# Kernel tuning notes

Measured on AMD Instinct MI355X. Metric: run time of the kernel, lower is better.

The kernel has to match this reference:

```python
import jax, jax.numpy as jnp
import numpy as np

NEG = -1000000.0  # mask fill value used by the torch module


def setup_inputs() -> dict:
    key = jax.random.key(0)
    k1, k2, k3, k4 = jax.random.split(key, 4)
    B, L, D = 64, 1024, 64
    return {
        "queries": jax.random.normal(k1, (B, L, D), dtype=jnp.float32),
        "keys": jax.random.normal(k2, (B, L, D), dtype=jnp.float32),
        "values": jax.random.normal(k3, (B, L, D), dtype=jnp.float32),
        "valid_lens": jax.random.randint(k4, (B,), 1, 1024, dtype=jnp.int32),
    }


def reference(queries, keys, values, valid_lens):
    d = queries.shape[-1]
    # [B, Lq, Lk] attention scores
    scores = jnp.einsum("bqd,bkd->bqk", queries, keys) / jnp.sqrt(jnp.asarray(d, queries.dtype))
    Lk = scores.shape[-1]
    # sequence mask: key positions >= valid_len are filled with NEG (per batch)
    col = jnp.arange(Lk)  # [Lk]
    mask = col[None, None, :] >= valid_lens[:, None, None]  # [B, 1, Lk] -> broadcasts over q
    scores = jnp.where(mask, NEG, scores)
    attn = jax.nn.softmax(scores, axis=-1)
    # dropout p=0.0 (eval) -> identity
    return jnp.einsum("bqk,bkd->bqd", attn, values)
```

## Files before the change

kernel.cpp:

```cpp
#include <hip/hip_runtime.h>
#include <math.h>


typedef __attribute__((ext_vector_type(4))) float f32x4;
typedef __attribute__((ext_vector_type(8))) short bf16x8;
typedef __attribute__((ext_vector_type(8))) unsigned short u16x8;
typedef __attribute__((ext_vector_type(4))) unsigned short u16x4;

constexpr int Bn = 64, Ln = 1024, Dn = 64;
constexpr float QSCALE = 0.125f * 1.44269504088896340736f;
constexpr float DEFER_THR = 10.0f;

__device__ inline unsigned short f2bf(float x) {
    unsigned int u = __float_as_uint(x);
    return (unsigned short)((u + 0x7fffu + ((u >> 16) & 1u)) >> 16);
}

__global__ __launch_bounds__(256) void flash_attn(
    const float* __restrict__ Q, const float* __restrict__ K,
    const float* __restrict__ V, const int* __restrict__ VL,
    float* __restrict__ O)
{
    __shared__ unsigned short kls[2][64 * 64];
    __shared__ unsigned short vls[2][64 * 64];
    __shared__ unsigned short plds[4][16 * 64];

    const int tid = threadIdx.x;
    const int w = tid >> 6, l = tid & 63;
    const int lg = l >> 4, ln = l & 15;
    const int b = blockIdx.x >> 4;
    const int qt = blockIdx.x & 15;
    const int qbase = qt * 64 + w * 16;
    const int valid = VL[b];
    const int nkt = (valid + 63) >> 6;

    const float* Kbase = K + (size_t)b * Ln * Dn;
    const float* Vbase = V + (size_t)b * Ln * Dn;

    bf16x8 bq0, bq1;
    {
        const f32x4* qp = reinterpret_cast<const f32x4*>(Q + ((size_t)b * Ln + qbase + ln) * Dn);
        f32x4 q0 = qp[lg * 2], q1 = qp[lg * 2 + 1], q2 = qp[8 + lg * 2], q3 = qp[8 + lg * 2 + 1];
        #pragma unroll
        for (int j = 0; j < 4; ++j) {
            bq0[j]     = (short)f2bf(q0[j] * QSCALE);
            bq0[j + 4] = (short)f2bf(q1[j] * QSCALE);
            bq1[j]     = (short)f2bf(q2[j] * QSCALE);
            bq1[j + 4] = (short)f2bf(q3[j] * QSCALE);
        }
    }

    const int kr = tid >> 2, kc = (tid & 3) * 16;
    const int vd = l, vk0 = w * 16;

    f32x4 kpre[4];
    float vpre[16];

    char* const kls0 = reinterpret_cast<char*>(kls[0]);
    char* const kls1 = reinterpret_cast<char*>(kls[1]);
    char* const vls0 = reinterpret_cast<char*>(vls[0]);
    char* const vls1 = reinterpret_cast<char*>(vls[1]);
    char* const pwb  = reinterpret_cast<char*>(plds[w]);

    const int kb = kr * 128 + kc * 2, ksw = (kr & 7) << 4;
    const int vb = vd * 128 + vk0 * 2, vsw = (vd & 7) << 4;

    auto stage_write = [&](int p) {
        char* kd = p ? kls1 : kls0;
        char* vd_ = p ? vls1 : vls0;
        u16x8 c0, c1;
        #pragma unroll
        for (int j = 0; j < 4; ++j) {
            c0[j]     = f2bf(kpre[0][j]);  c0[j + 4] = f2bf(kpre[1][j]);
            c1[j]     = f2bf(kpre[2][j]);  c1[j + 4] = f2bf(kpre[3][j]);
        }
        *reinterpret_cast<u16x8*>(kd + ((kb)      ^ ksw)) = c0;
        *reinterpret_cast<u16x8*>(kd + ((kb + 16) ^ ksw)) = c1;
        u16x8 v0, v1;
        #pragma unroll
        for (int j = 0; j < 8; ++j) { v0[j] = f2bf(vpre[j]); v1[j] = f2bf(vpre[j + 8]); }
        *reinterpret_cast<u16x8*>(vd_ + ((vb)      ^ vsw)) = v0;
        *reinterpret_cast<u16x8*>(vd_ + ((vb + 16) ^ vsw)) = v1;
    };

    {
        const f32x4* kp = reinterpret_cast<const f32x4*>(Kbase + (size_t)kr * Dn + kc);
        #pragma unroll
        for (int i = 0; i < 4; ++i) kpre[i] = kp[i];
        const float* vp = Vbase + (size_t)vk0 * Dn + vd;
        #pragma unroll
        for (int i = 0; i < 16; ++i) vpre[i] = vp[(size_t)i * Dn];
    }
    stage_write(0);
    __syncthreads();

    f32x4 acc[4] = {{0.f,0.f,0.f,0.f},{0.f,0.f,0.f,0.f},{0.f,0.f,0.f,0.f},{0.f,0.f,0.f,0.f}};
    float mrow = -1e30f;
    float lrow = 0.f;

    int p = 0;
    for (int kt = 0; kt < nkt; ++kt, p ^= 1) {
        const bool has_next = (kt + 1 < nkt);
        char* kcur = p ? kls1 : kls0;
        char* vcur = p ? vls1 : vls0;

        if (has_next) {
            const f32x4* kp = reinterpret_cast<const f32x4*>(Kbase + (size_t)((kt + 1) * 64 + kr) * Dn + kc);
            #pragma unroll
            for (int i = 0; i < 4; ++i) kpre[i] = kp[i];
            const float* vp = Vbase + (size_t)((kt + 1) * 64 + vk0) * Dn + vd;
            #pragma unroll
            for (int i = 0; i < 16; ++i) vpre[i] = vp[(size_t)i * Dn];
        }

        f32x4 st[4] = {{0.f,0.f,0.f,0.f},{0.f,0.f,0.f,0.f},{0.f,0.f,0.f,0.f},{0.f,0.f,0.f,0.f}};
        #pragma unroll
        for (int t = 0; t < 4; ++t) {
            const int r = 16 * t + ln, rsw = (r & 7) << 4;
            bf16x8 ak0 = *reinterpret_cast<const bf16x8*>(kcur + ((r * 128 + lg * 16)      ^ rsw));
            st[t] = __builtin_amdgcn_mfma_f32_16x16x32_bf16(ak0, bq0, st[t], 0, 0, 0);
            bf16x8 ak1 = *reinterpret_cast<const bf16x8*>(kcur + ((r * 128 + lg * 16 + 64) ^ rsw));
            st[t] = __builtin_amdgcn_mfma_f32_16x16x32_bf16(ak1, bq1, st[t], 0, 0, 0);
        }

        const int kb0 = kt * 64 + lg * 4;
        if (kt * 64 + 64 > valid) {
            #pragma unroll
            for (int t = 0; t < 4; ++t)
                #pragma unroll
                for (int j = 0; j < 4; ++j)
                    if (kb0 + 16 * t + j >= valid) st[t][j] = -1e30f;
        }

        float mx;
        {
            float a0 = fmaxf(fmaxf(st[0][0], st[0][1]), fmaxf(st[0][2], st[0][3]));
            float a1 = fmaxf(fmaxf(st[1][0], st[1][1]), fmaxf(st[1][2], st[1][3]));
            float a2 = fmaxf(fmaxf(st[2][0], st[2][1]), fmaxf(st[2][2], st[2][3]));
            float a3 = fmaxf(fmaxf(st[3][0], st[3][1]), fmaxf(st[3][2], st[3][3]));
            mx = fmaxf(fmaxf(a0, a1), fmaxf(a2, a3));
            mx = fmaxf(mx, __shfl_xor(mx, 16, 64));
            mx = fmaxf(mx, __shfl_xor(mx, 32, 64));
        }

        if (__any(mx - mrow > DEFER_THR)) {
            const float mn = fmaxf(mrow, mx);
            const float rs = exp2f(mrow - mn);
            mrow = mn;
            lrow *= rs;
            #pragma unroll
            for (int j = 0; j < 4; ++j) {
                const float rsj = __shfl(rs, lg * 4 + j, 64);
                #pragma unroll
                for (int t = 0; t < 4; ++t) acc[t][j] *= rsj;
            }
        }

        float rsum = 0.f;
        const int psw = (ln & 7) << 4;
        #pragma unroll
        for (int t = 0; t < 4; ++t) {
            u16x4 pk;
            #pragma unroll
            for (int j = 0; j < 4; ++j) {
                const float pv = exp2f(st[t][j] - mrow);
                rsum += pv;
                pk[j] = f2bf(pv);
            }
            *reinterpret_cast<u16x4*>(pwb + ((ln * 128 + 32 * t + 8 * lg) ^ psw)) = pk;
        }
        rsum += __shfl_xor(rsum, 16, 64);
        rsum += __shfl_xor(rsum, 32, 64);
        lrow += rsum;

        #pragma unroll
        for (int s = 0; s < 2; ++s) {
            bf16x8 pa = *reinterpret_cast<const bf16x8*>(pwb + ((ln * 128 + lg * 16 + 64 * s) ^ psw));
            #pragma unroll
            for (int t = 0; t < 4; ++t) {
                const int r = 16 * t + ln, rsw = (r & 7) << 4;
                bf16x8 bv = *reinterpret_cast<const bf16x8*>(vcur + ((r * 128 + lg * 16 + 64 * s) ^ rsw));
                acc[t] = __builtin_amdgcn_mfma_f32_16x16x32_bf16(pa, bv, acc[t], 0, 0, 0);
            }
        }

        if (has_next) stage_write(p ^ 1);
        __syncthreads();
    }

    const float invl = 1.0f / lrow;
    float inv[4];
    #pragma unroll
    for (int j = 0; j < 4; ++j) inv[j] = __shfl(invl, lg * 4 + j, 64);
    float* Orow = O + ((size_t)b * Ln + qbase) * Dn;
    #pragma unroll
    for (int t = 0; t < 4; ++t) {
        #pragma unroll
        for (int j = 0; j < 4; ++j) {
            const int q = lg * 4 + j;
            const int d = 16 * t + ln;
            Orow[(size_t)q * Dn + d] = acc[t][j] * inv[j];
        }
    }
}

extern "C" void kernel_launch(void* const* d_in, const int* in_sizes, int n_in,
                              void* d_out, int out_size, void* d_ws, size_t ws_size,
                              hipStream_t stream) {
    const float* Q = (const float*)d_in[0];
    const float* K = (const float*)d_in[1];
    const float* V = (const float*)d_in[2];
    const int* VL = (const int*)d_in[3];
    float* O = (float*)d_out;
    flash_attn<<<Bn * 16, 256, 0, stream>>>(Q, K, V, VL, O);
}
```

Measured before the change: 127.2 us.

## Schedule batches longest-first and permute K rows for wider P stores

Each block ranks the 64 batches by valid length using wave shuffles and maps blockIdx through a scrambled permutation, so the longest batches start first and the variable-length tail is balanced across CUs. Separately, K rows are written to shared memory with a permuted row order, so each lane's score outputs become key-contiguous. That allows the P tile to be written with two 128-bit LDS stores instead of four 64-bit ones, and the mask index is updated to match. The cost is a per-block 64-iteration ranking loop and an extra barrier at kernel start.

New measurement: 137.5 us. 1.08x slower.

```diff
diff --git a/kernel.cpp b/kernel.cpp
--- a/kernel.cpp
+++ b/kernel.cpp
@@ -5,7 +5,6 @@
 typedef __attribute__((ext_vector_type(4))) float f32x4;
 typedef __attribute__((ext_vector_type(8))) short bf16x8;
 typedef __attribute__((ext_vector_type(8))) unsigned short u16x8;
-typedef __attribute__((ext_vector_type(4))) unsigned short u16x4;
 
 constexpr int Bn = 64, Ln = 1024, Dn = 64;
 constexpr float QSCALE = 0.125f * 1.44269504088896340736f;
@@ -24,12 +23,26 @@
     __shared__ unsigned short kls[2][64 * 64];
     __shared__ unsigned short vls[2][64 * 64];
     __shared__ unsigned short plds[4][16 * 64];
+    __shared__ int order_s[64];
 
     const int tid = threadIdx.x;
     const int w = tid >> 6, l = tid & 63;
     const int lg = l >> 4, ln = l & 15;
-    const int b = blockIdx.x >> 4;
-    const int qt = blockIdx.x & 15;
+
+    {
+        const int vme = VL[l];
+        int rank = 0;
+        for (int i = 0; i < 64; ++i) {
+            const int vi = __shfl(vme, i, 64);
+            rank += (vi > vme) || (vi == vme && i < l);
+        }
+        if (w == 0) order_s[rank] = l;
+    }
+    __syncthreads();
+
+    const int r = (633 * blockIdx.x) & 1023;
+    const int b = order_s[r >> 4];
+    const int qt = r & 15;
     const int qbase = qt * 64 + w * 16;
     const int valid = VL[b];
     const int nkt = (valid + 63) >> 6;
@@ -51,6 +64,7 @@
     }
 
     const int kr = tid >> 2, kc = (tid & 3) * 16;
+    const int sr = ((kr & 0xC) << 2) | ((kr >> 2) & 0xC) | (kr & 3);
     const int vd = l, vk0 = w * 16;
 
     f32x4 kpre[4];
@@ -62,12 +76,13 @@
     char* const vls1 = reinterpret_cast<char*>(vls[1]);
     char* const pwb  = reinterpret_cast<char*>(plds[w]);
 
-    const int kb = kr * 128 + kc * 2, ksw = (kr & 7) << 4;
+    const int kb = sr * 128 + kc * 2, ksw = (sr & 7) << 4;
     const int vb = vd * 128 + vk0 * 2, vsw = (vd & 7) << 4;
-
-    auto stage_write = [&](int p) {
-        char* kd = p ? kls1 : kls0;
-        char* vd_ = p ? vls1 : vls0;
+    const int psw = (ln & 7) << 4;
+
+    auto stage_write = [&](int pbuf) {
+        char* kd = pbuf ? kls1 : kls0;
+        char* vdst = pbuf ? vls1 : vls0;
         u16x8 c0, c1;
         #pragma unroll
         for (int j = 0; j < 4; ++j) {
@@ -79,8 +94,8 @@
         u16x8 v0, v1;
         #pragma unroll
         for (int j = 0; j < 8; ++j) { v0[j] = f2bf(vpre[j]); v1[j] = f2bf(vpre[j + 8]); }
-        *reinterpret_cast<u16x8*>(vd_ + ((vb)      ^ vsw)) = v0;
-        *reinterpret_cast<u16x8*>(vd_ + ((vb + 16) ^ vsw)) = v1;
+        *reinterpret_cast<u16x8*>(vdst + ((vb)      ^ vsw)) = v0;
+        *reinterpret_cast<u16x8*>(vdst + ((vb + 16) ^ vsw)) = v1;
     };
 
     {
@@ -116,20 +131,19 @@
         f32x4 st[4] = {{0.f,0.f,0.f,0.f},{0.f,0.f,0.f,0.f},{0.f,0.f,0.f,0.f},{0.f,0.f,0.f,0.f}};
         #pragma unroll
         for (int t = 0; t < 4; ++t) {
-            const int r = 16 * t + ln, rsw = (r & 7) << 4;
-            bf16x8 ak0 = *reinterpret_cast<const bf16x8*>(kcur + ((r * 128 + lg * 16)      ^ rsw));
+            const int rr = 16 * t + ln, rsw = (rr & 7) << 4;
+            bf16x8 ak0 = *reinterpret_cast<const bf16x8*>(kcur + ((rr * 128 + lg * 16)      ^ rsw));
             st[t] = __builtin_amdgcn_mfma_f32_16x16x32_bf16(ak0, bq0, st[t], 0, 0, 0);
-            bf16x8 ak1 = *reinterpret_cast<const bf16x8*>(kcur + ((r * 128 + lg * 16 + 64) ^ rsw));
+            bf16x8 ak1 = *reinterpret_cast<const bf16x8*>(kcur + ((rr * 128 + lg * 16 + 64) ^ rsw));
             st[t] = __builtin_amdgcn_mfma_f32_16x16x32_bf16(ak1, bq1, st[t], 0, 0, 0);
         }
 
-        const int kb0 = kt * 64 + lg * 4;
         if (kt * 64 + 64 > valid) {
             #pragma unroll
             for (int t = 0; t < 4; ++t)
                 #pragma unroll
                 for (int j = 0; j < 4; ++j)
-                    if (kb0 + 16 * t + j >= valid) st[t][j] = -1e30f;
+                    if (kt * 64 + 16 * lg + 4 * t + j >= valid) st[t][j] = -1e30f;
         }
 
         float mx;
@@ -157,18 +171,25 @@
         }
 
         float rsum = 0.f;
-        const int psw = (ln & 7) << 4;
-        #pragma unroll
-        for (int t = 0; t < 4; ++t) {
-            u16x4 pk;
+        u16x8 plo, phi;
+        #pragma unroll
+        for (int t = 0; t < 2; ++t)
             #pragma unroll
             for (int j = 0; j < 4; ++j) {
                 const float pv = exp2f(st[t][j] - mrow);
                 rsum += pv;
-                pk[j] = f2bf(pv);
-            }
-            *reinterpret_cast<u16x4*>(pwb + ((ln * 128 + 32 * t + 8 * lg) ^ psw)) = pk;
-        }
+                plo[t * 4 + j] = f2bf(pv);
+            }
+        #pragma unroll
+        for (int t = 2; t < 4; ++t)
+            #pragma unroll
+            for (int j = 0; j < 4; ++j) {
+                const float pv = exp2f(st[t][j] - mrow);
+                rsum += pv;
+                phi[(t - 2) * 4 + j] = f2bf(pv);
+            }
+        *reinterpret_cast<u16x8*>(pwb + ((ln * 128 + 32 * lg)      ^ psw)) = plo;
+        *reinterpret_cast<u16x8*>(pwb + ((ln * 128 + 32 * lg + 16) ^ psw)) = phi;
         rsum += __shfl_xor(rsum, 16, 64);
         rsum += __shfl_xor(rsum, 32, 64);
         lrow += rsum;
@@ -178,8 +199,8 @@
             bf16x8 pa = *reinterpret_cast<const bf16x8*>(pwb + ((ln * 128 + lg * 16 + 64 * s) ^ psw));
             #pragma unroll
             for (int t = 0; t < 4; ++t) {
-                const int r = 16 * t + ln, rsw = (r & 7) << 4;
-                bf16x8 bv = *reinterpret_cast<const bf16x8*>(vcur + ((r * 128 + lg * 16 + 64 * s) ^ rsw));
+                const int rr = 16 * t + ln, rsw = (rr & 7) << 4;
+                bf16x8 bv = *reinterpret_cast<const bf16x8*>(vcur + ((rr * 128 + lg * 16 + 64 * s) ^ rsw));
                 acc[t] = __builtin_amdgcn_mfma_f32_16x16x32_bf16(pa, bv, acc[t], 0, 0, 0);
             }
         }
```
